# Performance work log

Hardware: AMD Instinct MI355X
Metric: run time of the kernel (lower is better)

Reference implementation:

```python
import jax, jax.numpy as jnp
import numpy as np

N_HEADS = 8
EMBED_DIM = 64  # per-head dim


def setup_inputs() -> dict:
    key = jax.random.key(0)
    k1, k2, k3 = jax.random.split(key, 3)
    B, S, F = 2, 2048, 512
    x = jax.random.normal(k1, (B, S, F), dtype=jnp.float32)
    W = jax.random.normal(k2, (F, EMBED_DIM * N_HEADS * 3), dtype=jnp.float32) * 0.02
    b = jax.random.normal(k3, (EMBED_DIM * N_HEADS * 3,), dtype=jnp.float32) * 0.02
    return {"x": x, "W": W, "b": b}


def reference(x, W, b):
    B, S, F = x.shape
    H, E = N_HEADS, EMBED_DIM
    emb = x @ W + b                                   # (B, S, E*H*3)
    heads = emb.reshape(B, S, E, H, 3)
    heads = jnp.transpose(heads, (0, 4, 3, 1, 2))     # (B, 3, H, S, E)
    q, k, v = heads[:, 0], heads[:, 1], heads[:, 2]   # each (B, H, S, E)
    qk = jnp.einsum('bhse,bhte->bhst', q, k)          # (B, H, S, S)
    # Original multiplies softmax by `scaling` then divides by it -> exact cancel.
    # Note: no scaling applied BEFORE softmax in the source (faithful).
    attn = jax.nn.softmax(qk, axis=-1)
    out = jnp.einsum('bhst,bhte->bhse', attn, v)      # (B, H, S, E)
    out = jnp.transpose(out, (0, 2, 1, 3)).reshape(B, S, H * E)
    return out
```

## Files before the change

kernel.cpp:

```cpp
#include <hip/hip_runtime.h>


using half8  = __attribute__((ext_vector_type(8))) _Float16;
using f32x4  = __attribute__((ext_vector_type(4))) float;
using float4v = __attribute__((ext_vector_type(4))) float;
using uint2v = __attribute__((ext_vector_type(2))) unsigned int;
using uint4v = __attribute__((ext_vector_type(4))) unsigned int;

constexpr int BN = 2, HN = 8, SN = 2048, EN = 64, FN = 512;
constexpr size_t T_ELEMS = (size_t)BN * HN * SN * EN;

constexpr size_t WB_BYTES = (size_t)24 * 16 * 4 * 64 * 8 * 2;
constexpr size_t BP_OFF   = WB_BYTES;
constexpr size_t VT_OFF   = BP_OFF + 1536 * 4;
constexpr size_t VT_BYTES = T_ELEMS * 2;
constexpr size_t QKV_OFF  = VT_OFF + VT_BYTES;

__device__ inline unsigned int pack2h(float a, float b) {
  auto h = __builtin_amdgcn_cvt_pkrtz(a, b);
  return __builtin_bit_cast(unsigned int, h);
}

__device__ __forceinline__ void async_copy16(void* lds, const void* g) {
  __builtin_amdgcn_global_load_lds(
      (const __attribute__((address_space(1))) unsigned int*)g,
      (__attribute__((address_space(3))) unsigned int*)lds, 16, 0, 0);
}

__global__ __launch_bounds__(256) void repack_kernel(
    const float* __restrict__ W, const float* __restrict__ bias,
    _Float16* __restrict__ Wb, float* __restrict__ bp) {
  int t = blockIdx.x * 256 + threadIdx.x;
  int lane = t & 63;
  int cb = (t >> 6) & 3;
  int kc = (t >> 8) & 15;
  int ch = t >> 12;
  int e = cb * 16 + (lane & 15);
  int fb = kc * 32 + (lane >> 4) * 8;
  int c = ch >> 3, h = ch & 7;
  int j = e * 24 + h * 3 + c;
  half8 o;
  #pragma unroll
  for (int i = 0; i < 8; ++i) o[i] = (_Float16)W[(size_t)(fb + i) * 1536 + j];
  *(half8*)(Wb + (size_t)t * 8) = o;
  if (t < 1536) {
    int cc = t % 3, hh = (t / 3) & 7, ee = t / 24;
    bp[(cc * 8 + hh) * 64 + ee] = bias[t];
  }
}

__global__ __launch_bounds__(256) void proj_kernel(
    const float* __restrict__ x, const _Float16* __restrict__ Wb,
    const float* __restrict__ bp, _Float16* __restrict__ qkv,
    _Float16* __restrict__ vt) {
  __shared__ _Float16 tl[64 * 72];
  int rt = blockIdx.x, cg = blockIdx.y;
  int wave = threadIdx.x >> 6, lane = threadIdx.x & 63;
  int lcol = lane & 15, lg = lane >> 4;
  int row0 = rt * 64 + wave * 16;
  f32x4 acc[3][4] = {};
  const float* xr = x + (size_t)(row0 + lcol) * FN;
  for (int kc = 0; kc < 16; ++kc) {
    const float4v* xp = (const float4v*)(xr + kc * 32 + lg * 8);
    float4v x0 = xp[0], x1 = xp[1];
    half8 a;
    #pragma unroll
    for (int i = 0; i < 4; ++i) { a[i] = (_Float16)x0[i]; a[4 + i] = (_Float16)x1[i]; }
    #pragma unroll
    for (int chi = 0; chi < 3; ++chi) {
      int ch = cg * 3 + chi;
      #pragma unroll
      for (int cb = 0; cb < 4; ++cb) {
        half8 bfr = *(const half8*)(Wb + ((((size_t)ch * 16 + kc) * 4 + cb) * 64 + lane) * 8);
        acc[chi][cb] = __builtin_amdgcn_mfma_f32_16x16x32_f16(a, bfr, acc[chi][cb], 0, 0, 0);
      }
    }
  }
  int b = rt >> 5, s0 = (rt & 31) * 64;
  #pragma unroll
  for (int chi = 0; chi < 3; ++chi) {
    int ch = cg * 3 + chi;
    int c = ch >> 3, h = ch & 7;
    if (c < 2) {
      _Float16* dst = qkv + (size_t)c * T_ELEMS;
      #pragma unroll
      for (int cb = 0; cb < 4; ++cb) {
        int e = cb * 16 + lcol;
        float bv = bp[ch * 64 + e];
        #pragma unroll
        for (int r = 0; r < 4; ++r) {
          int s = s0 + wave * 16 + lg * 4 + r;
          dst[((size_t)(b * HN + h) * SN + s) * EN + e] = (_Float16)(acc[chi][cb][r] + bv);
        }
      }
    } else {
      #pragma unroll
      for (int cb = 0; cb < 4; ++cb) {
        int e = cb * 16 + lcol;
        float bv = bp[ch * 64 + e];
        #pragma unroll
        for (int r = 0; r < 4; ++r)
          tl[(wave * 16 + lg * 4 + r) * 72 + e] = (_Float16)(acc[chi][cb][r] + bv);
      }
      __syncthreads();
      int e = threadIdx.x >> 2, sc = threadIdx.x & 3;
      half8 o0, o1;
      #pragma unroll
      for (int i = 0; i < 8; ++i) o0[i] = tl[(sc * 16 + i) * 72 + e];
      #pragma unroll
      for (int i = 0; i < 8; ++i) o1[i] = tl[(sc * 16 + 8 + i) * 72 + e];
      _Float16* dstv = vt + ((size_t)(b * HN + h) * EN + e) * SN + s0 + sc * 16;
      *(half8*)dstv = o0;
      *(half8*)(dstv + 8) = o1;
      __syncthreads();
    }
  }
}

__global__ __launch_bounds__(256, 2) void attn_kernel(
    const _Float16* __restrict__ q_ws, const _Float16* __restrict__ k_ws,
    const _Float16* __restrict__ vt_ws, float* __restrict__ out) {
  __shared__ __align__(16) char smem[57344];

  int bid = blockIdx.x;
  int lb = (bid & 7) * 64 + (bid >> 3);
  int bh = lb >> 5, qblk = lb & 31;
  int wave = threadIdx.x >> 6, lane = threadIdx.x & 63;
  int q = lane & 15, g = lane >> 4;
  int q0 = qblk * 64 + wave * 16;

  const _Float16* qb  = q_ws  + ((size_t)bh * SN + q0) * EN;
  const _Float16* kb  = k_ws  + (size_t)bh * SN * EN;
  const _Float16* vtb = vt_ws + (size_t)bh * EN * SN;

  half8 qf[2];
  qf[0] = *(const half8*)(qb + (size_t)q * EN + g * 8);
  qf[1] = *(const half8*)(qb + (size_t)q * EN + 32 + g * 8);

  f32x4 o[4] = {};
  float m = -3e38f, l = 0.f;
  unsigned int* pw = (unsigned int*)(smem + 49152 + wave * 2048);

  int sub = lane >> 3;
  int off8 = ((lane & 7) ^ sub) * 8;
  int lin = lane * 16;

  auto stage = [&](int c, int t) {
    char* kbuf = smem + c * 16384;
    char* vbuf = kbuf + 8192;
    int kv = t * 64;
    #pragma unroll
    for (int ii = 0; ii < 2; ++ii) {
      int i = wave * 2 + ii;
      int row = i * 8 + sub;
      async_copy16(kbuf + i * 1024 + lin, kb + (size_t)(kv + row) * EN + off8);
      async_copy16(vbuf + i * 1024 + lin, vtb + (size_t)row * SN + kv + off8);
    }
  };

  int qx = (q & 7) << 4;

  auto compute = [&](int c) {
    const char* kbuf = smem + c * 16384;
    const char* vbuf = kbuf + 8192;
    half8 kf[4][2], vf[4][2];
    #pragma unroll
    for (int kt = 0; kt < 4; ++kt)
      #pragma unroll
      for (int eh = 0; eh < 2; ++eh)
        kf[kt][eh] = *(const half8*)(kbuf + ((((kt * 16 + q) * 128) + eh * 64 + g * 16) ^ qx));
    #pragma unroll
    for (int et = 0; et < 4; ++et)
      #pragma unroll
      for (int kh = 0; kh < 2; ++kh)
        vf[et][kh] = *(const half8*)(vbuf + ((((et * 16 + q) * 128) + kh * 64 + g * 16) ^ qx));

    f32x4 s[4];
    f32x4 z = {};
    __builtin_amdgcn_s_setprio(1);
    #pragma unroll
    for (int kt = 0; kt < 4; ++kt) {
      s[kt] = __builtin_amdgcn_mfma_f32_16x16x32_f16(kf[kt][0], qf[0], z, 0, 0, 0);
      s[kt] = __builtin_amdgcn_mfma_f32_16x16x32_f16(kf[kt][1], qf[1], s[kt], 0, 0, 0);
    }
    __builtin_amdgcn_s_setprio(0);

    float mx = s[0][0];
    #pragma unroll
    for (int kt = 0; kt < 4; ++kt)
      #pragma unroll
      for (int r = 0; r < 4; ++r) mx = fmaxf(mx, s[kt][r]);
    mx = fmaxf(mx, __shfl_xor(mx, 16));
    mx = fmaxf(mx, __shfl_xor(mx, 32));
    if (!__all(mx <= m + 8.f)) {
      float mn = fmaxf(m, mx);
      float scl = __expf(m - mn);
      m = mn;
      l *= scl;
      #pragma unroll
      for (int et = 0; et < 4; ++et)
        #pragma unroll
        for (int r = 0; r < 4; ++r) o[et][r] *= scl;
    }
    float ps = 0.f;
    #pragma unroll
    for (int kt = 0; kt < 4; ++kt) {
      float p0 = __expf(s[kt][0] - m), p1 = __expf(s[kt][1] - m);
      float p2 = __expf(s[kt][2] - m), p3 = __expf(s[kt][3] - m);
      ps += (p0 + p1) + (p2 + p3);
      uint2v wv;
      wv.x = pack2h(p0, p1);
      wv.y = pack2h(p2, p3);
      int w = kt * 8 + 2 * g;
      int phys = (((w >> 2) + q) & 7) * 4 + (w & 3);
      *(uint2v*)&pw[q * 32 + phys] = wv;
    }
    l += ps;
    asm volatile("s_waitcnt lgkmcnt(0)" ::: "memory");
    __builtin_amdgcn_sched_barrier(0);
    half8 pf[2];
    #pragma unroll
    for (int kh = 0; kh < 2; ++kh) {
      int cc = kh * 4 + g;
      uint4v tv = *(const uint4v*)&pw[q * 32 + ((cc + q) & 7) * 4];
      pf[kh] = __builtin_bit_cast(half8, tv);
    }
    __builtin_amdgcn_sched_barrier(0);
    __builtin_amdgcn_s_setprio(1);
    #pragma unroll
    for (int et = 0; et < 4; ++et) {
      o[et] = __builtin_amdgcn_mfma_f32_16x16x32_f16(vf[et][0], pf[0], o[et], 0, 0, 0);
      o[et] = __builtin_amdgcn_mfma_f32_16x16x32_f16(vf[et][1], pf[1], o[et], 0, 0, 0);
    }
    __builtin_amdgcn_s_setprio(0);
  };

  stage(0, 0);
  stage(1, 1);
  for (int t = 0; t < 31; ++t) {
    asm volatile("s_waitcnt vmcnt(4)" ::: "memory");
    __syncthreads();
    if (t + 2 < 32) stage((t + 2) % 3, t + 2);
    compute(t % 3);
  }
  asm volatile("s_waitcnt vmcnt(0)" ::: "memory");
  __syncthreads();
  compute(31 % 3);

  l += __shfl_xor(l, 16);
  l += __shfl_xor(l, 32);
  float rl = 1.f / l;
  int b = bh >> 3, h = bh & 7;
  float* ow = (float*)(smem + wave * 4096);
  #pragma unroll
  for (int et = 0; et < 4; ++et)
    #pragma unroll
    for (int r = 0; r < 4; ++r) {
      int e = et * 16 + g * 4 + r;
      ow[q * 64 + ((e + q * 4) & 63)] = o[et][r] * rl;
    }
  asm volatile("s_waitcnt lgkmcnt(0)" ::: "memory");
  __builtin_amdgcn_sched_barrier(0);
  #pragma unroll
  for (int qr = 0; qr < 16; ++qr) {
    float vvv = ow[qr * 64 + ((lane + qr * 4) & 63)];
    out[((size_t)b * SN + q0 + qr) * 512 + h * 64 + lane] = vvv;
  }
}

extern "C" void kernel_launch(void* const* d_in, const int* in_sizes, int n_in,
                              void* d_out, int out_size, void* d_ws, size_t ws_size,
                              hipStream_t stream) {
  const float* x    = (const float*)d_in[0];
  const float* W    = (const float*)d_in[1];
  const float* bias = (const float*)d_in[2];
  float* out = (float*)d_out;
  char* ws = (char*)d_ws;
  _Float16* Wb  = (_Float16*)(ws);
  float*    bp  = (float*)(ws + BP_OFF);
  _Float16* vt  = (_Float16*)(ws + VT_OFF);
  _Float16* qkv = (_Float16*)(ws + QKV_OFF);

  repack_kernel<<<384, 256, 0, stream>>>(W, bias, Wb, bp);
  proj_kernel<<<dim3(64, 8), 256, 0, stream>>>(x, Wb, bp, qkv, vt);
  attn_kernel<<<512, 256, 0, stream>>>(qkv, qkv + T_ELEMS, vt, out);
}
```

Measured before the change: 133.4 us.

## Rewrite QKV projection as LDS-tiled double-buffered GEMM with fp16 pre-converted x

The prep kernel now converts x to fp16 and lays W out N-major (row per output column, K contiguous), alongside the permuted bias. The projection becomes a 128x128 tiled GEMM that stages A and B tiles into swizzled LDS with async global-to-LDS copies, double-buffered over K, and each wave computes a 64x64 sub-tile. This raises data reuse compared with the earlier per-wave 16-row scheme, which read W from global memory with no sharing between waves. In exchange it adds an extra fp16 copy of x in workspace. The V transpose also changes: it now uses direct strided half4 stores instead of an LDS transpose.

```diff
diff --git a/kernel.cpp b/kernel.cpp
--- a/kernel.cpp
+++ b/kernel.cpp
@@ -1,6 +1,7 @@
 #include <hip/hip_runtime.h>
 
 
+using half4v = __attribute__((ext_vector_type(4))) _Float16;
 using half8  = __attribute__((ext_vector_type(8))) _Float16;
 using f32x4  = __attribute__((ext_vector_type(4))) float;
 using float4v = __attribute__((ext_vector_type(4))) float;
@@ -10,9 +11,11 @@
 constexpr int BN = 2, HN = 8, SN = 2048, EN = 64, FN = 512;
 constexpr size_t T_ELEMS = (size_t)BN * HN * SN * EN;
 
-constexpr size_t WB_BYTES = (size_t)24 * 16 * 4 * 64 * 8 * 2;
-constexpr size_t BP_OFF   = WB_BYTES;
-constexpr size_t VT_OFF   = BP_OFF + 1536 * 4;
+constexpr size_t WD_BYTES = (size_t)1536 * 512 * 2;
+constexpr size_t BPN_OFF  = WD_BYTES;
+constexpr size_t X16_OFF  = BPN_OFF + 1536 * 4;
+constexpr size_t X16_BYTES = (size_t)4096 * 512 * 2;
+constexpr size_t VT_OFF   = X16_OFF + X16_BYTES;
 constexpr size_t VT_BYTES = T_ELEMS * 2;
 constexpr size_t QKV_OFF  = VT_OFF + VT_BYTES;
 
@@ -27,92 +30,134 @@
       (__attribute__((address_space(3))) unsigned int*)lds, 16, 0, 0);
 }
 
-__global__ __launch_bounds__(256) void repack_kernel(
-    const float* __restrict__ W, const float* __restrict__ bias,
-    _Float16* __restrict__ Wb, float* __restrict__ bp) {
+__global__ __launch_bounds__(256) void prep_kernel(
+    const float* __restrict__ x, const float* __restrict__ W,
+    const float* __restrict__ bias, _Float16* __restrict__ x16,
+    _Float16* __restrict__ Wd, float* __restrict__ bpn) {
   int t = blockIdx.x * 256 + threadIdx.x;
-  int lane = t & 63;
-  int cb = (t >> 6) & 3;
-  int kc = (t >> 8) & 15;
-  int ch = t >> 12;
-  int e = cb * 16 + (lane & 15);
-  int fb = kc * 32 + (lane >> 4) * 8;
-  int c = ch >> 3, h = ch & 7;
-  int j = e * 24 + h * 3 + c;
+  const float4v* src = (const float4v*)(x + (size_t)t * 8);
+  float4v a = src[0], b = src[1];
   half8 o;
   #pragma unroll
-  for (int i = 0; i < 8; ++i) o[i] = (_Float16)W[(size_t)(fb + i) * 1536 + j];
-  *(half8*)(Wb + (size_t)t * 8) = o;
+  for (int i = 0; i < 4; ++i) { o[i] = (_Float16)a[i]; o[4 + i] = (_Float16)b[i]; }
+  *(half8*)(x16 + (size_t)t * 8) = o;
+
+  if (t < 1536 * 64) {
+    int n = t >> 6, cc = t & 63, fb = cc * 8;
+    int ch = n >> 6, e = n & 63, c = ch >> 3, h = ch & 7;
+    int j = e * 24 + h * 3 + c;
+    half8 w;
+    #pragma unroll
+    for (int i = 0; i < 8; ++i) w[i] = (_Float16)W[(size_t)(fb + i) * 1536 + j];
+    *(half8*)(Wd + (size_t)n * 512 + fb) = w;
+  }
   if (t < 1536) {
-    int cc = t % 3, hh = (t / 3) & 7, ee = t / 24;
-    bp[(cc * 8 + hh) * 64 + ee] = bias[t];
-  }
-}
-
-__global__ __launch_bounds__(256) void proj_kernel(
-    const float* __restrict__ x, const _Float16* __restrict__ Wb,
-    const float* __restrict__ bp, _Float16* __restrict__ qkv,
+    int ch = t >> 6, e = t & 63, c = ch >> 3, h = ch & 7;
+    bpn[t] = bias[e * 24 + h * 3 + c];
+  }
+}
+
+__global__ __launch_bounds__(256, 2) void proj_kernel(
+    const _Float16* __restrict__ x16, const _Float16* __restrict__ Wd,
+    const float* __restrict__ bpn, _Float16* __restrict__ qkv,
     _Float16* __restrict__ vt) {
-  __shared__ _Float16 tl[64 * 72];
-  int rt = blockIdx.x, cg = blockIdx.y;
-  int wave = threadIdx.x >> 6, lane = threadIdx.x & 63;
-  int lcol = lane & 15, lg = lane >> 4;
-  int row0 = rt * 64 + wave * 16;
-  f32x4 acc[3][4] = {};
-  const float* xr = x + (size_t)(row0 + lcol) * FN;
-  for (int kc = 0; kc < 16; ++kc) {
-    const float4v* xp = (const float4v*)(xr + kc * 32 + lg * 8);
-    float4v x0 = xp[0], x1 = xp[1];
-    half8 a;
-    #pragma unroll
-    for (int i = 0; i < 4; ++i) { a[i] = (_Float16)x0[i]; a[4 + i] = (_Float16)x1[i]; }
-    #pragma unroll
-    for (int chi = 0; chi < 3; ++chi) {
-      int ch = cg * 3 + chi;
-      #pragma unroll
-      for (int cb = 0; cb < 4; ++cb) {
-        half8 bfr = *(const half8*)(Wb + ((((size_t)ch * 16 + kc) * 4 + cb) * 64 + lane) * 8);
-        acc[chi][cb] = __builtin_amdgcn_mfma_f32_16x16x32_f16(a, bfr, acc[chi][cb], 0, 0, 0);
+  __shared__ __align__(16) char smem[65536];
+
+  int tid = threadIdx.x;
+  int wave = tid >> 6, lane = tid & 63;
+  int q16 = lane & 15, g = lane >> 4;
+  int wm = wave >> 1, wn = wave & 1;
+  int gm_blk = blockIdx.x * 128, gn_blk = blockIdx.y * 128;
+
+  f32x4 acc[4][4] = {};
+
+  auto stage = [&](int c, int ks) {
+    char* Ab = smem + c * 16384;
+    char* Bb = smem + 32768 + c * 16384;
+    int k0 = ks * 64;
+    #pragma unroll
+    for (int ii = 0; ii < 4; ++ii) {
+      int qq = tid + 256 * ii;
+      int row = qq >> 3, cc = qq & 7;
+      int sc = (cc ^ (row & 7)) * 8;
+      async_copy16(Ab + qq * 16, x16 + (size_t)(gm_blk + row) * 512 + k0 + sc);
+      async_copy16(Bb + qq * 16, Wd + (size_t)(gn_blk + row) * 512 + k0 + sc);
+    }
+  };
+
+  auto compute = [&](int c) {
+    const char* Ab = smem + c * 16384;
+    const char* Bb = smem + 32768 + c * 16384;
+    #pragma unroll
+    for (int kh = 0; kh < 2; ++kh) {
+      half8 af[4], bf[4];
+      #pragma unroll
+      for (int mt = 0; mt < 4; ++mt) {
+        int m = wm * 64 + mt * 16 + q16;
+        af[mt] = *(const half8*)(Ab + m * 128 + ((kh * 64 + g * 16) ^ ((m & 7) << 4)));
       }
-    }
-  }
-  int b = rt >> 5, s0 = (rt & 31) * 64;
+      #pragma unroll
+      for (int nt = 0; nt < 4; ++nt) {
+        int n = wn * 64 + nt * 16 + q16;
+        bf[nt] = *(const half8*)(Bb + n * 128 + ((kh * 64 + g * 16) ^ ((n & 7) << 4)));
+      }
+      __builtin_amdgcn_s_setprio(1);
+      #pragma unroll
+      for (int mt = 0; mt < 4; ++mt)
+        #pragma unroll
+        for (int nt = 0; nt < 4; ++nt)
+          acc[mt][nt] = __builtin_amdgcn_mfma_f32_16x16x32_f16(af[mt], bf[nt], acc[mt][nt], 0, 0, 0);
+      __builtin_amdgcn_s_setprio(0);
+    }
+  };
+
+  stage(0, 0);
   #pragma unroll
-  for (int chi = 0; chi < 3; ++chi) {
-    int ch = cg * 3 + chi;
-    int c = ch >> 3, h = ch & 7;
-    if (c < 2) {
-      _Float16* dst = qkv + (size_t)c * T_ELEMS;
-      #pragma unroll
-      for (int cb = 0; cb < 4; ++cb) {
-        int e = cb * 16 + lcol;
-        float bv = bp[ch * 64 + e];
+  for (int ks = 0; ks < 8; ++ks) {
+    int cur = ks & 1;
+    __syncthreads();
+    if (ks + 1 < 8) {
+      stage(cur ^ 1, ks + 1);
+      asm volatile("s_waitcnt vmcnt(8)" ::: "memory");
+    } else {
+      asm volatile("s_waitcnt vmcnt(0)" ::: "memory");
+    }
+    __syncthreads();
+    compute(cur);
+  }
+
+  int gn0 = gn_blk + wn * 64;
+  int ch = gn0 >> 6, c = ch >> 3, h = ch & 7;
+  int gm0 = gm_blk + wm * 64;
+  if (c < 2) {
+    _Float16* dst = qkv + (size_t)c * T_ELEMS;
+    #pragma unroll
+    for (int nt = 0; nt < 4; ++nt) {
+      int e = nt * 16 + q16;
+      float bv = bpn[gn0 + nt * 16 + q16];
+      #pragma unroll
+      for (int mt = 0; mt < 4; ++mt)
         #pragma unroll
         for (int r = 0; r < 4; ++r) {
-          int s = s0 + wave * 16 + lg * 4 + r;
-          dst[((size_t)(b * HN + h) * SN + s) * EN + e] = (_Float16)(acc[chi][cb][r] + bv);
+          int gm = gm0 + mt * 16 + g * 4 + r;
+          int b = gm >> 11, s = gm & 2047;
+          dst[((size_t)(b * HN + h) * SN + s) * EN + e] = (_Float16)(acc[mt][nt][r] + bv);
         }
+    }
+  } else {
+    #pragma unroll
+    for (int nt = 0; nt < 4; ++nt) {
+      int e = nt * 16 + q16;
+      float bv = bpn[gn0 + nt * 16 + q16];
+      #pragma unroll
+      for (int mt = 0; mt < 4; ++mt) {
+        int gm = gm0 + mt * 16 + g * 4;
+        int b = gm >> 11, s = gm & 2047;
+        half4v hv;
+        #pragma unroll
+        for (int r = 0; r < 4; ++r) hv[r] = (_Float16)(acc[mt][nt][r] + bv);
+        *(half4v*)(vt + ((size_t)(b * HN + h) * EN + e) * SN + s) = hv;
       }
-    } else {
-      #pragma unroll
-      for (int cb = 0; cb < 4; ++cb) {
-        int e = cb * 16 + lcol;
-        float bv = bp[ch * 64 + e];
-        #pragma unroll
-        for (int r = 0; r < 4; ++r)
-          tl[(wave * 16 + lg * 4 + r) * 72 + e] = (_Float16)(acc[chi][cb][r] + bv);
-      }
-      __syncthreads();
-      int e = threadIdx.x >> 2, sc = threadIdx.x & 3;
-      half8 o0, o1;
-      #pragma unroll
-      for (int i = 0; i < 8; ++i) o0[i] = tl[(sc * 16 + i) * 72 + e];
-      #pragma unroll
-      for (int i = 0; i < 8; ++i) o1[i] = tl[(sc * 16 + 8 + i) * 72 + e];
-      _Float16* dstv = vt + ((size_t)(b * HN + h) * EN + e) * SN + s0 + sc * 16;
-      *(half8*)dstv = o0;
-      *(half8*)(dstv + 8) = o1;
-      __syncthreads();
     }
   }
 }
@@ -276,12 +321,13 @@
   const float* bias = (const float*)d_in[2];
   float* out = (float*)d_out;
   char* ws = (char*)d_ws;
-  _Float16* Wb  = (_Float16*)(ws);
-  float*    bp  = (float*)(ws + BP_OFF);
+  _Float16* Wd  = (_Float16*)(ws);
+  float*    bpn = (float*)(ws + BPN_OFF);
+  _Float16* x16 = (_Float16*)(ws + X16_OFF);
   _Float16* vt  = (_Float16*)(ws + VT_OFF);
   _Float16* qkv = (_Float16*)(ws + QKV_OFF);
 
-  repack_kernel<<<384, 256, 0, stream>>>(W, bias, Wb, bp);
-  proj_kernel<<<dim3(64, 8), 256, 0, stream>>>(x, Wb, bp, qkv, vt);
+  prep_kernel<<<1024, 256, 0, stream>>>(x, W, bias, x16, Wd, bpn);
+  proj_kernel<<<dim3(32, 12), 256, 0, stream>>>(x16, Wd, bpn, qkv, vt);
   attn_kernel<<<512, 256, 0, stream>>>(qkv, qkv + T_ELEMS, vt, out);
 }
```

Measured after the change: 120.1 us. -10.0%, faster.
